# Performance work log

Hardware: AMD Instinct MI355X
Metric: run time of the kernel (lower is better)

## Reference

```python
import jax, jax.numpy as jnp
import numpy as np

D_MODEL = 256
NUM_HEADS = 8
WINDOW = 7
B, H, W = 2, 56, 56


def setup_inputs() -> dict:
    key = jax.random.key(0)
    ks = jax.random.split(key, 9)
    s = D_MODEL ** -0.5
    return {
        "x": jax.random.normal(ks[0], (B, D_MODEL, H, W), jnp.float32),
        "wq": jax.random.normal(ks[1], (D_MODEL, D_MODEL), jnp.float32) * s,
        "bq": jnp.zeros((D_MODEL,), jnp.float32),
        "wk": jax.random.normal(ks[2], (D_MODEL, D_MODEL), jnp.float32) * s,
        "bk": jnp.zeros((D_MODEL,), jnp.float32),
        "wv": jax.random.normal(ks[3], (D_MODEL, D_MODEL), jnp.float32) * s,
        "bv": jnp.zeros((D_MODEL,), jnp.float32),
        "wo": jax.random.normal(ks[4], (D_MODEL, D_MODEL), jnp.float32) * s,
        "bo": jnp.zeros((D_MODEL,), jnp.float32),
    }


def _proj(x, w, b):
    # 1x1 conv == channel matmul. x: [B,C,H,W], w: [Cout,Cin], b: [Cout]
    return jnp.einsum('oc,bchw->bohw', w, x) + b[None, :, None, None]


def _windows(t, ws):
    # t: [B,h,d,H,W] -> [B,h,d,H,W,ws*ws], zero-padded sliding windows.
    # Row-major (i*ws + j) flattening matches torch unfold(3).unfold(4).view(...,-1).
    pad = ws // 2
    Hh, Ww = t.shape[-2], t.shape[-1]
    tp = jnp.pad(t, ((0, 0), (0, 0), (0, 0), (pad, pad), (pad, pad)))
    return jnp.stack([tp[..., i:i + Hh, j:j + Ww]
                      for i in range(ws) for j in range(ws)], axis=-1)


def reference(x, wq, bq, wk, bk, wv, bv, wo, bo):
    Bt, C, Hh, Ww = x.shape
    hd = C // NUM_HEADS
    scale = hd ** -0.5
    q = _proj(x, wq, bq).reshape(Bt, NUM_HEADS, hd, Hh, Ww)
    k = _proj(x, wk, bk).reshape(Bt, NUM_HEADS, hd, Hh, Ww)
    v = _proj(x, wv, bv).reshape(Bt, NUM_HEADS, hd, Hh, Ww)
    kw = _windows(k, WINDOW)  # [B,h,d,H,W,ws^2]
    vw = _windows(v, WINDOW)
    attn = jnp.einsum('bhdxy,bhdxyw->bhxyw', q, kw) * scale
    attn = jax.nn.softmax(attn, axis=-1)
    out = jnp.einsum('bhxyw,bhdxyw->bhdxy', attn, vw).reshape(Bt, C, Hh, Ww)
    return _proj(out, wo, bo)
```

## Files before the change

### kernel.cpp

```cpp
#include <hip/hip_runtime.h>
#include <cstdint>

#define NHEAD 8
#define HD 32
#define DM 256
#define HH 56
#define WWID 56
#define HW 3136
#define NB 2
#define SCALE 0.17677669529663687f

#if __has_builtin(__builtin_amdgcn_exp2f)
#define QSCALE 0.25503488f
#define EXPW(x) __builtin_amdgcn_exp2f(x)
#else
#define QSCALE SCALE
#define EXPW(x) __expf(x)
#endif

typedef _Float16 f16;
typedef __attribute__((ext_vector_type(2))) _Float16 f16x2;
typedef __attribute__((ext_vector_type(8))) _Float16 f16x8;
typedef __attribute__((ext_vector_type(4))) float floatx4;

union U16 { uint4 u; f16x2 h2[4]; f16 h[8]; };

#define GLD16(g, l) __builtin_amdgcn_global_load_lds( \
    (__attribute__((address_space(1))) void*)(g),     \
    (__attribute__((address_space(3))) void*)(l), 16, 0, 0)

#if __has_builtin(__builtin_amdgcn_update_dpp)
__device__ __forceinline__ float quad_sum(float s) {
    float t1 = __int_as_float(__builtin_amdgcn_update_dpp(
        0, __float_as_int(s), 0xB1, 0xF, 0xF, true));
    s += t1;
    float t2 = __int_as_float(__builtin_amdgcn_update_dpp(
        0, __float_as_int(s), 0x4E, 0xF, 0xF, true));
    return s + t2;
}
#else
__device__ __forceinline__ float quad_sum(float s) {
    s += __shfl_xor(s, 1);
    s += __shfl_xor(s, 2);
    return s;
}
#endif

__device__ __forceinline__ float dot8(const U16& a, const U16& b) {
    float s = __builtin_amdgcn_fdot2(a.h2[0], b.h2[0], 0.0f, false);
    s = __builtin_amdgcn_fdot2(a.h2[1], b.h2[1], s, false);
    s = __builtin_amdgcn_fdot2(a.h2[2], b.h2[2], s, false);
    s = __builtin_amdgcn_fdot2(a.h2[3], b.h2[3], s, false);
    return s;
}

__global__ __launch_bounds__(256) void prep(
    const float* __restrict__ x,
    const float* __restrict__ wq, const float* __restrict__ wk,
    const float* __restrict__ wv, const float* __restrict__ wo,
    f16* __restrict__ xT, f16* __restrict__ wcat, f16* __restrict__ wob)
{
    const int bid = blockIdx.x;
    const int t = threadIdx.x;
    if (bid < 1568) {
        __shared__ float tile[32][33];
        const int b = bid / 784, r = bid - 784 * b;
        const int ct = r / 98;
        const int p0 = (r - ct * 98) * 32, c0 = ct * 32;
        const int tx = t & 31, ty = t >> 5;
        const float* xb = x + (size_t)b * DM * HW;
        #pragma unroll
        for (int i = 0; i < 4; ++i)
            tile[ty + i * 8][tx] = xb[(size_t)(c0 + ty + i * 8) * HW + p0 + tx];
        __syncthreads();
        f16* xo = xT + (size_t)b * HW * DM;
        #pragma unroll
        for (int i = 0; i < 4; ++i)
            xo[(size_t)(p0 + ty + i * 8) * DM + c0 + tx] =
                (f16)tile[tx][ty + i * 8];
    } else {
        const int gid = (bid - 1568) * 256 + t;
        const int idx4 = gid << 2;
        const int sel = idx4 >> 16;
        const int off = idx4 & 65535;
        const float* src = sel == 0 ? wq : (sel == 1 ? wk : (sel == 2 ? wv : wo));
        f16* dst = sel < 3 ? (wcat + (sel << 16) + off) : (wob + off);
        float4 f = *(const float4*)&src[off];
        union { ushort4 u; f16 h[4]; } pk;
        pk.h[0] = (f16)f.x; pk.h[1] = (f16)f.y;
        pk.h[2] = (f16)f.z; pk.h[3] = (f16)f.w;
        *(ushort4*)dst = pk.u;
    }
}

template<int MODE>
__global__ __launch_bounds__(256) void gemm_mfma(
    const f16* __restrict__ A,
    const f16* __restrict__ Bm,
    const float* __restrict__ b0, const float* __restrict__ b1,
    const float* __restrict__ b2,
    void* __restrict__ o0, void* __restrict__ o1, void* __restrict__ o2)
{
    const int bb = blockIdx.z;
    const int n0 = blockIdx.x * 64;
    const int m0 = blockIdx.y * 128;
    const f16* Bb = Bm + (size_t)bb * HW * DM + (size_t)n0 * DM;

    __shared__ __align__(16) f16 As[2][128][32];
    __shared__ __align__(16) f16 Bs[2][64][32];

    const int t = threadIdx.x;
    const int wave = t >> 6, lane = t & 63;
    const int quad = lane >> 4, l16 = lane & 15;
    const int mw = (wave & 1) * 64, nw = (wave >> 1) * 32;

    floatx4 acc[4][2] = {};

    const int sr = t >> 2;
    const int sq = (t & 3) << 3;
    const f16* gA = A + (size_t)(m0 + sr) * DM + sq;
    const f16* gB = Bb + (size_t)sr * DM + sq;
    f16* lA[2]  = { &As[0][sr][sq],      &As[1][sr][sq]      };
    f16* lA2[2] = { &As[0][sr + 64][sq], &As[1][sr + 64][sq] };
    f16* lB[2]  = { &Bs[0][sr][sq],      &Bs[1][sr][sq]      };

    GLD16(gA, lA[0]);
    GLD16(gA + 64 * DM, lA2[0]);
    GLD16(gB, lB[0]);

    #pragma unroll
    for (int kk = 0; kk < 8; ++kk) {
        const int cur = kk & 1, nxt = cur ^ 1;
        if (kk < 7) {
            const int ko = (kk + 1) * 32;
            GLD16(gA + ko, lA[nxt]);
            GLD16(gA + 64 * DM + ko, lA2[nxt]);
            GLD16(gB + ko, lB[nxt]);
            asm volatile("s_waitcnt vmcnt(3)" ::: "memory");
        } else {
            asm volatile("s_waitcnt vmcnt(0)" ::: "memory");
        }
        __builtin_amdgcn_s_barrier();
        __builtin_amdgcn_sched_barrier(0);
        f16x8 af[4], bf[2];
        #pragma unroll
        for (int mt = 0; mt < 4; ++mt)
            af[mt] = *(const f16x8*)&As[cur][mw + mt * 16 + l16][quad * 8];
        #pragma unroll
        for (int nt = 0; nt < 2; ++nt)
            bf[nt] = *(const f16x8*)&Bs[cur][nw + nt * 16 + l16][quad * 8];
        #pragma unroll
        for (int mt = 0; mt < 4; ++mt)
            #pragma unroll
            for (int nt = 0; nt < 2; ++nt)
                acc[mt][nt] = __builtin_amdgcn_mfma_f32_16x16x32_f16(
                    af[mt], bf[nt], acc[mt][nt], 0, 0, 0);
        asm volatile("s_waitcnt lgkmcnt(0)" ::: "memory");
        __builtin_amdgcn_sched_barrier(0);
        __builtin_amdgcn_s_barrier();
    }

    if (MODE == 0) {
        #pragma unroll
        for (int mt = 0; mt < 4; ++mt) {
            const int gm = m0 + mw + mt * 16 + quad * 4;
            const int proj = gm >> 8;
            const int c = gm & 255;
            const int h = c >> 5, d0 = c & 31;
            const float* bptr = proj == 0 ? b0 : (proj == 1 ? b1 : b2);
            f16* op = (f16*)(proj == 0 ? o0 : (proj == 1 ? o1 : o2));
            const float sc = proj == 0 ? QSCALE : 1.0f;
            const size_t base = ((size_t)(bb * NHEAD + h) * HW) * HD + d0;
            float bias[4] = {bptr[c], bptr[c + 1], bptr[c + 2], bptr[c + 3]};
            #pragma unroll
            for (int nt = 0; nt < 2; ++nt) {
                const int p = n0 + nw + nt * 16 + l16;
                union { ushort4 u; f16 h[4]; } pk;
                #pragma unroll
                for (int r = 0; r < 4; ++r)
                    pk.h[r] = (f16)((acc[mt][nt][r] + bias[r]) * sc);
                *(ushort4*)&op[base + (size_t)p * HD] = pk.u;
            }
        }
    } else {
        float* yo = (float*)o0;
        #pragma unroll
        for (int mt = 0; mt < 4; ++mt) {
            const int gc = m0 + mw + mt * 16 + quad * 4;
            #pragma unroll
            for (int r = 0; r < 4; ++r) {
                const float bias = b0[gc + r];
                #pragma unroll
                for (int nt = 0; nt < 2; ++nt) {
                    const int p = n0 + nw + nt * 16 + l16;
                    yo[(size_t)(bb * DM + gc + r) * HW + p] = acc[mt][nt][r] + bias;
                }
            }
        }
    }
}

#define HROWS 8
#define HPOS  (HROWS * WWID)
#define HPP   (HPOS + 6)

__global__ __launch_bounds__(224) void attn_win(
    const f16* __restrict__ q,
    const f16* __restrict__ k,
    const f16* __restrict__ v,
    f16* __restrict__ out)
{
    __shared__ uint4 kh[HPP * 4];
    __shared__ uint4 vh[HPP * 4];

    const int t = threadIdx.x;
    const int tile = blockIdx.x;
    const int h = blockIdx.y, b = blockIdx.z;
    const int y0 = tile * 2;
    const size_t base = (size_t)(b * NHEAD + h) * HW * HD;
    const f16* kp = k + base;
    const f16* vp = v + base;

    #pragma unroll
    for (int it = 0; it < 8; ++it) {
        const int u = t + it * 224;
        const int pos = u >> 2, ch = u & 3;
        const int hr = pos / WWID;
        const int gx = pos - hr * WWID;
        const int gy = y0 - 3 + hr;
        uint4 kv = make_uint4(0, 0, 0, 0), vv = make_uint4(0, 0, 0, 0);
        if ((unsigned)gy < HH) {
            const size_t g = (size_t)(gy * WWID + gx) * HD + (ch << 3);
            kv = *(const uint4*)&kp[g];
            vv = *(const uint4*)&vp[g];
        }
        kh[u + 12] = kv;
        vh[u + 12] = vv;
    }
    if (t < 48) {
        const int ps = t % 6;
        const int fi = (ps < 3 ? ps * 4 : (HPOS + ps) * 4) + ((t / 6) & 3);
        const uint4 z = make_uint4(0, 0, 0, 0);
        if (t < 24) kh[fi] = z; else vh[fi] = z;
    }
    __syncthreads();

    const int g  = t >> 2;
    const int ch = t & 3;
    const int ry = g >= 28 ? 1 : 0;
    const int px = g - ry * 28;
    const int x0 = px * 2;
    const int plA = ry * WWID + x0;
    const int pA = y0 * WWID + plA;
    const int tA = plA * 4 + ch;

    U16 qa, qb;
    qa.u = *(const uint4*)(q + base + (size_t)pA * HD + (ch << 3));
    qb.u = *(const uint4*)(q + base + (size_t)(pA + 1) * HD + (ch << 3));

    const uint4* kb4 = kh + tA;
    const uint4* vb4 = vh + tA;

    float inr[8];
    float cA = 0.f, cB = 0.f;
    #pragma unroll
    for (int c = 0; c < 8; ++c) {
        inr[c] = ((unsigned)(x0 + c - 3) < WWID) ? 1.0f : 0.0f;
        if (c < 7) cA += inr[c];
        if (c > 0) cB += inr[c];
    }
    float ofA[8] = {}, ofB[8] = {};
    float sumA = 7.0f * (7.0f - cA);
    float sumB = 7.0f * (7.0f - cB);

    for (int i = 0; i < 7; ++i) {
        #pragma unroll
        for (int c = 0; c < 8; ++c) {
            const int off4 = (i * WWID + c) << 2;
            U16 ku; ku.u = kb4[off4];
            U16 vu; vu.u = vb4[off4];
            if (c < 7) {
                float s = quad_sum(dot8(ku, qa));
                const float w = EXPW(s) * inr[c];
                sumA += w;
                #pragma unroll
                for (int n = 0; n < 8; ++n)
                    ofA[n] = fmaf((float)vu.h[n], w, ofA[n]);
            }
            if (c > 0) {
                float s = quad_sum(dot8(ku, qb));
                const float w = EXPW(s) * inr[c];
                sumB += w;
                #pragma unroll
                for (int n = 0; n < 8; ++n)
                    ofB[n] = fmaf((float)vu.h[n], w, ofB[n]);
            }
        }
    }

#if __has_builtin(__builtin_amdgcn_rcpf)
    const float invA = __builtin_amdgcn_rcpf(sumA);
    const float invB = __builtin_amdgcn_rcpf(sumB);
#else
    const float invA = 1.0f / sumA;
    const float invB = 1.0f / sumB;
#endif
    f16* opA = out + ((size_t)b * HW + pA) * DM + h * HD + (ch << 3);
    f16* opB = opA + DM;
    U16 oa, ob;
    #pragma unroll
    for (int n = 0; n < 8; ++n) {
        oa.h[n] = (f16)(ofA[n] * invA);
        ob.h[n] = (f16)(ofB[n] * invB);
    }
    *(uint4*)opA = oa.u;
    *(uint4*)opB = ob.u;
}

extern "C" void kernel_launch(void* const* d_in, const int* in_sizes, int n_in,
                              void* d_out, int out_size, void* d_ws, size_t ws_size,
                              hipStream_t stream) {
    const float* x  = (const float*)d_in[0];
    const float* wq = (const float*)d_in[1];
    const float* bq = (const float*)d_in[2];
    const float* wk = (const float*)d_in[3];
    const float* bk = (const float*)d_in[4];
    const float* wv = (const float*)d_in[5];
    const float* bv = (const float*)d_in[6];
    const float* wo = (const float*)d_in[7];
    const float* bo = (const float*)d_in[8];
    float* out = (float*)d_out;

    const size_t NPC = (size_t)NB * HW * DM;
    f16* xT    = (f16*)d_ws;
    f16* wcat  = xT + NPC;
    f16* wob   = wcat + 768 * 256;
    f16* qb    = wob + 256 * 256;
    f16* kb    = qb + NPC;
    f16* vb    = kb + NPC;
    f16* attnT = vb + NPC;

    prep<<<1824, 256, 0, stream>>>(x, wq, wk, wv, wo, xT, wcat, wob);
    gemm_mfma<0><<<dim3(HW / 64, 6, NB), 256, 0, stream>>>(
        wcat, xT, bq, bk, bv, qb, kb, vb);
    attn_win<<<dim3(28, NHEAD, NB), 224, 0, stream>>>(qb, kb, vb, attnT);
    gemm_mfma<1><<<dim3(HW / 64, 2, NB), 256, 0, stream>>>(
        wob, attnT, bo, bo, bo, out, out, out);
}
```

Baseline: 105.5 us.

## Deepen GEMM K-stage, enlarge attention row tile, use direct-to-LDS halo loads

The GEMM now stages 64 K-elements per pipeline step instead of 32, which halves the barrier count and doubles the bytes in flight. The attention kernel now covers 4 output rows per block with 448 threads, so the 6-row K/V halo is shared across more rows. Its halo fill uses direct global-to-LDS loads, with out-of-range rows redirected to a zero buffer that prep clears. The cost is more LDS per block and only 224 attention blocks, which may lower occupancy and parallelism.

Result: faster. 103.4 us, median of 2 (-2.0%).

```diff
diff --git a/kernel.cpp b/kernel.cpp
--- a/kernel.cpp
+++ b/kernel.cpp
@@ -58,7 +58,8 @@
     const float* __restrict__ x,
     const float* __restrict__ wq, const float* __restrict__ wk,
     const float* __restrict__ wv, const float* __restrict__ wo,
-    f16* __restrict__ xT, f16* __restrict__ wcat, f16* __restrict__ wob)
+    f16* __restrict__ xT, f16* __restrict__ wcat, f16* __restrict__ wob,
+    f16* __restrict__ zbuf)
 {
     const int bid = blockIdx.x;
     const int t = threadIdx.x;
@@ -79,6 +80,8 @@
             xo[(size_t)(p0 + ty + i * 8) * DM + c0 + tx] =
                 (f16)tile[tx][ty + i * 8];
     } else {
+        if (bid == 1823 && t < 4)
+            ((uint4*)zbuf)[t] = make_uint4(0, 0, 0, 0);
         const int gid = (bid - 1568) * 256 + t;
         const int idx4 = gid << 2;
         const int sel = idx4 >> 16;
@@ -106,8 +109,8 @@
     const int m0 = blockIdx.y * 128;
     const f16* Bb = Bm + (size_t)bb * HW * DM + (size_t)n0 * DM;
 
-    __shared__ __align__(16) f16 As[2][128][32];
-    __shared__ __align__(16) f16 Bs[2][64][32];
+    __shared__ __align__(16) f16 As[2][2][128][32];
+    __shared__ __align__(16) f16 Bs[2][2][64][32];
 
     const int t = threadIdx.x;
     const int wave = t >> 6, lane = t & 63;
@@ -120,45 +123,50 @@
     const int sq = (t & 3) << 3;
     const f16* gA = A + (size_t)(m0 + sr) * DM + sq;
     const f16* gB = Bb + (size_t)sr * DM + sq;
-    f16* lA[2]  = { &As[0][sr][sq],      &As[1][sr][sq]      };
-    f16* lA2[2] = { &As[0][sr + 64][sq], &As[1][sr + 64][sq] };
-    f16* lB[2]  = { &Bs[0][sr][sq],      &Bs[1][sr][sq]      };
-
-    GLD16(gA, lA[0]);
-    GLD16(gA + 64 * DM, lA2[0]);
-    GLD16(gB, lB[0]);
+
+#define STAGE(buf, k0)                                           \
+    GLD16(gA + (k0),                 &As[buf][0][sr][sq]);       \
+    GLD16(gA + 64 * DM + (k0),       &As[buf][0][sr + 64][sq]);  \
+    GLD16(gA + (k0) + 32,            &As[buf][1][sr][sq]);       \
+    GLD16(gA + 64 * DM + (k0) + 32,  &As[buf][1][sr + 64][sq]);  \
+    GLD16(gB + (k0),                 &Bs[buf][0][sr][sq]);       \
+    GLD16(gB + (k0) + 32,            &Bs[buf][1][sr][sq]);
+
+    STAGE(0, 0)
 
     #pragma unroll
-    for (int kk = 0; kk < 8; ++kk) {
-        const int cur = kk & 1, nxt = cur ^ 1;
-        if (kk < 7) {
-            const int ko = (kk + 1) * 32;
-            GLD16(gA + ko, lA[nxt]);
-            GLD16(gA + 64 * DM + ko, lA2[nxt]);
-            GLD16(gB + ko, lB[nxt]);
-            asm volatile("s_waitcnt vmcnt(3)" ::: "memory");
+    for (int kk = 0; kk < 4; ++kk) {
+        const int cur = kk & 1;
+        if (kk < 3) {
+            const int ko = (kk + 1) * 64;
+            if (cur == 0) { STAGE(1, ko) } else { STAGE(0, ko) }
+            asm volatile("s_waitcnt vmcnt(6)" ::: "memory");
         } else {
             asm volatile("s_waitcnt vmcnt(0)" ::: "memory");
         }
         __builtin_amdgcn_s_barrier();
         __builtin_amdgcn_sched_barrier(0);
-        f16x8 af[4], bf[2];
-        #pragma unroll
-        for (int mt = 0; mt < 4; ++mt)
-            af[mt] = *(const f16x8*)&As[cur][mw + mt * 16 + l16][quad * 8];
-        #pragma unroll
-        for (int nt = 0; nt < 2; ++nt)
-            bf[nt] = *(const f16x8*)&Bs[cur][nw + nt * 16 + l16][quad * 8];
-        #pragma unroll
-        for (int mt = 0; mt < 4; ++mt)
+        #pragma unroll
+        for (int s = 0; s < 2; ++s) {
+            f16x8 af[4], bf[2];
+            #pragma unroll
+            for (int mt = 0; mt < 4; ++mt)
+                af[mt] = *(const f16x8*)&As[cur][s][mw + mt * 16 + l16][quad * 8];
             #pragma unroll
             for (int nt = 0; nt < 2; ++nt)
-                acc[mt][nt] = __builtin_amdgcn_mfma_f32_16x16x32_f16(
-                    af[mt], bf[nt], acc[mt][nt], 0, 0, 0);
+                bf[nt] = *(const f16x8*)&Bs[cur][s][nw + nt * 16 + l16][quad * 8];
+            #pragma unroll
+            for (int mt = 0; mt < 4; ++mt)
+                #pragma unroll
+                for (int nt = 0; nt < 2; ++nt)
+                    acc[mt][nt] = __builtin_amdgcn_mfma_f32_16x16x32_f16(
+                        af[mt], bf[nt], acc[mt][nt], 0, 0, 0);
+        }
         asm volatile("s_waitcnt lgkmcnt(0)" ::: "memory");
         __builtin_amdgcn_sched_barrier(0);
         __builtin_amdgcn_s_barrier();
     }
+#undef STAGE
 
     if (MODE == 0) {
         #pragma unroll
@@ -200,15 +208,16 @@
     }
 }
 
-#define HROWS 8
+#define HROWS 10
 #define HPOS  (HROWS * WWID)
 #define HPP   (HPOS + 6)
 
-__global__ __launch_bounds__(224) void attn_win(
+__global__ __launch_bounds__(448) void attn_win(
     const f16* __restrict__ q,
     const f16* __restrict__ k,
     const f16* __restrict__ v,
-    f16* __restrict__ out)
+    f16* __restrict__ out,
+    const f16* __restrict__ zbuf)
 {
     __shared__ uint4 kh[HPP * 4];
     __shared__ uint4 vh[HPP * 4];
@@ -216,26 +225,24 @@
     const int t = threadIdx.x;
     const int tile = blockIdx.x;
     const int h = blockIdx.y, b = blockIdx.z;
-    const int y0 = tile * 2;
+    const int y0 = tile * 4;
     const size_t base = (size_t)(b * NHEAD + h) * HW * HD;
     const f16* kp = k + base;
     const f16* vp = v + base;
 
     #pragma unroll
-    for (int it = 0; it < 8; ++it) {
-        const int u = t + it * 224;
+    for (int it = 0; it < 5; ++it) {
+        const int u = t + it * 448;
         const int pos = u >> 2, ch = u & 3;
         const int hr = pos / WWID;
         const int gx = pos - hr * WWID;
         const int gy = y0 - 3 + hr;
-        uint4 kv = make_uint4(0, 0, 0, 0), vv = make_uint4(0, 0, 0, 0);
-        if ((unsigned)gy < HH) {
-            const size_t g = (size_t)(gy * WWID + gx) * HD + (ch << 3);
-            kv = *(const uint4*)&kp[g];
-            vv = *(const uint4*)&vp[g];
-        }
-        kh[u + 12] = kv;
-        vh[u + 12] = vv;
+        const bool val = (unsigned)gy < HH;
+        const size_t g = (size_t)(gy * WWID + gx) * HD + (ch << 3);
+        const f16* ks = val ? kp + g : zbuf;
+        const f16* vs = val ? vp + g : zbuf;
+        GLD16(ks, (f16*)&kh[u + 12]);
+        GLD16(vs, (f16*)&vh[u + 12]);
     }
     if (t < 48) {
         const int ps = t % 6;
@@ -247,7 +254,7 @@
 
     const int g  = t >> 2;
     const int ch = t & 3;
-    const int ry = g >= 28 ? 1 : 0;
+    const int ry = g / 28;
     const int px = g - ry * 28;
     const int x0 = px * 2;
     const int plA = ry * WWID + x0;
@@ -339,11 +346,12 @@
     f16* kb    = qb + NPC;
     f16* vb    = kb + NPC;
     f16* attnT = vb + NPC;
-
-    prep<<<1824, 256, 0, stream>>>(x, wq, wk, wv, wo, xT, wcat, wob);
+    f16* zbuf  = attnT + NPC;
+
+    prep<<<1824, 256, 0, stream>>>(x, wq, wk, wv, wo, xT, wcat, wob, zbuf);
     gemm_mfma<0><<<dim3(HW / 64, 6, NB), 256, 0, stream>>>(
         wcat, xT, bq, bk, bv, qb, kb, vb);
-    attn_win<<<dim3(28, NHEAD, NB), 224, 0, stream>>>(qb, kb, vb, attnT);
+    attn_win<<<dim3(14, NHEAD, NB), 448, 0, stream>>>(qb, kb, vb, attnT, zbuf);
     gemm_mfma<1><<<dim3(HW / 64, 2, NB), 256, 0, stream>>>(
         wob, attnT, bo, bo, bo, out, out, out);
 }
```
